# Performance work log

Hardware: AMD Instinct MI355X
Metric: run time of the kernel (lower is better)

The kernel has to match this reference:

```python
import jax, jax.numpy as jnp
import numpy as np

B, DX, DY = 64, 1024, 10

def setup_inputs() -> dict:
    key = jax.random.key(0)
    k1, k2 = jax.random.split(key)
    inputs = jax.random.normal(k1, (B, DX, DX), dtype=jnp.float32)
    rho = jax.random.normal(k2, (DX, DY, DX, DY), dtype=jnp.float32)
    return {"inputs": inputs, "rho": rho}

def reference(inputs, rho):
    # Original: rho_res = einsum('bik,klmn,bmo->bilon', inputs, rho, inputs)
    #           trace   = einsum('bijij->b', rho_res)   (full trace of rank-5 tensor)
    #           rho_y   = einsum('bijik->bjk', rho_res / trace)  (partial trace)
    # Equivalent without materializing the rank-5 intermediate:
    #   rho_y_un[b,j,k] = sum_{i,p,m} inputs[b,i,p] rho[p,j,m,k] inputs[b,m,i]
    #                   = sum_{m,p} (inputs @ inputs)[b,m,p] rho[p,j,m,k]
    #   trace[b] = sum_j rho_y_un[b,j,j]  (partial trace commutes with full trace)
    A = jnp.einsum('bmi,bip->bmp', inputs, inputs)          # [B, DX, DX]
    rho_y = jnp.einsum('bmp,pjmk->bjk', A, rho)             # [B, DY, DY]
    trace = jnp.trace(rho_y, axis1=-2, axis2=-1)            # [B]
    return rho_y / trace[:, None, None]
```

## Files before the change

kernel.cpp:

```cpp
#include <hip/hip_runtime.h>
#include <stdint.h>

#define DX 1024
#define NB 64
#define DY 10
#define NJK 100

typedef unsigned short ushort_t;
typedef __attribute__((ext_vector_type(8))) short short8;
typedef __attribute__((ext_vector_type(4))) float f32x4;
typedef __attribute__((ext_vector_type(16))) float f32x16;

#define VMCNT6 asm volatile("s_waitcnt vmcnt(6)" ::: "memory")
#define VMCNT5 asm volatile("s_waitcnt vmcnt(5)" ::: "memory")
#define VMCNT4 asm volatile("s_waitcnt vmcnt(4)" ::: "memory")
#define VMCNT0 asm volatile("s_waitcnt vmcnt(0)" ::: "memory")
#define LGKM0 asm volatile("s_waitcnt lgkmcnt(0)" ::: "memory")
#define CFENCE asm volatile("" ::: "memory")

__device__ __forceinline__ unsigned short f2bf(float f) {
  unsigned int u = __builtin_bit_cast(unsigned int, f);
  u += 0x7fffu + ((u >> 16) & 1u);
  return (unsigned short)(u >> 16);
}
__device__ __forceinline__ float bf2f(unsigned short h) {
  unsigned int u = ((unsigned int)h) << 16;
  return __builtin_bit_cast(float, u);
}
__device__ __forceinline__ void gload16(const void* g, void* l) {
  __builtin_amdgcn_global_load_lds((const __attribute__((address_space(1))) unsigned int*)g,
                                   (__attribute__((address_space(3))) unsigned int*)l, 16, 0, 0);
}

__launch_bounds__(256)
__global__ void p0_rho(const float* __restrict__ rho, ushort_t* __restrict__ R2,
                       float* __restrict__ S) {
  __shared__ ushort_t R_s[112 * 128];
  int p = blockIdx.x;
  int t = threadIdx.x;
  const float* rp = rho + (size_t)p * (DY * DX * DY);
  ushort_t* R2p = R2 + (size_t)p * (112 * 1024);
  int m = t >> 1, h = t & 1;

  for (int mc = 0; mc < 8; ++mc) {
    __syncthreads();
    float ssum = 0.f;
#pragma unroll
    for (int j = 0; j < DY; ++j) {
      const float* bj = rp + (size_t)j * (DX * DY) + (size_t)(mc * 128 + m) * DY;
      const float4 q = *(const float4*)(bj + h * 4);
      const float e = bj[8 + h];
      int rb = j * DY + h * 4;
      R_s[((rb + 0) * 128 + m) ^ (((rb + 0) & 15) << 3)] = f2bf(q.x);
      R_s[((rb + 1) * 128 + m) ^ (((rb + 1) & 15) << 3)] = f2bf(q.y);
      R_s[((rb + 2) * 128 + m) ^ (((rb + 2) & 15) << 3)] = f2bf(q.z);
      R_s[((rb + 3) * 128 + m) ^ (((rb + 3) & 15) << 3)] = f2bf(q.w);
      int r8 = j * DY + 8 + h;
      R_s[(r8 * 128 + m) ^ ((r8 & 15) << 3)] = f2bf(e);
      if (h == 0) {
        if (j == 0) ssum += q.x;
        if (j == 1) ssum += q.y;
        if (j == 2) ssum += q.z;
        if (j == 3) ssum += q.w;
        if (j == 8) ssum += e;
      } else {
        if (j == 4) ssum += q.x;
        if (j == 5) ssum += q.y;
        if (j == 6) ssum += q.z;
        if (j == 7) ssum += q.w;
        if (j == 9) ssum += e;
      }
    }
    ssum += __shfl_xor(ssum, 1, 64);
    if (h == 0) S[(size_t)p * DX + mc * 128 + m] = ssum;
    __syncthreads();
#pragma unroll
    for (int i = 0; i < 7; ++i) {
      int c = i * 256 + t;
      int row = c >> 4, sl = c & 15;
      uint4 v = make_uint4(0u, 0u, 0u, 0u);
      if (row < NJK) v = *(const uint4*)&R_s[(row * 128 + sl * 8) ^ ((row & 15) << 3)];
      *(uint4*)(R2p + (size_t)row * 1024 + mc * 128 + sl * 8) = v;
    }
  }
}

__launch_bounds__(256)
__global__ void p0_split(const float* __restrict__ X,
                         ushort_t* __restrict__ XHL, ushort_t* __restrict__ XtHL) {
  __shared__ float T[64][65];
  int blk = blockIdx.x;
  int bl = blk >> 8;
  int tt = blk & 255;
  int r0 = (tt >> 4) << 6;
  int c0 = (tt & 15) << 6;
  const float* Xb = X + (size_t)bl * DX * DX;
  int t = threadIdx.x;
  int r = t >> 4, c = t & 15;
#pragma unroll
  for (int s = 0; s < 4; ++s) {
    const float4 v = *(const float4*)(Xb + (size_t)(r0 + r + 16 * s) * DX + c0 + c * 4);
    T[r + 16 * s][c * 4 + 0] = v.x;
    T[r + 16 * s][c * 4 + 1] = v.y;
    T[r + 16 * s][c * 4 + 2] = v.z;
    T[r + 16 * s][c * 4 + 3] = v.w;
  }
  __syncthreads();
  int s8 = t & 7;
  int rw = t >> 3;
  int isLo = s8 >> 2, q = s8 & 3;
#pragma unroll
  for (int ktl = 0; ktl < 2; ++ktl) {
#pragma unroll
    for (int sp = 0; sp < 2; ++sp) {
      int loc = rw + sp * 32;
      {
        unsigned short hh8[8];
#pragma unroll
        for (int e = 0; e < 8; ++e) {
          float x = T[loc][ktl * 32 + q * 8 + e];
          unsigned short hh = f2bf(x);
          hh8[e] = isLo ? f2bf(x - bf2f(hh)) : hh;
        }
        int kt = (c0 >> 5) + ktl;
        size_t off = (((size_t)bl * 32 + kt) * 1024 + (r0 + loc)) * 64 + s8 * 8;
        uint4 v;
        v.x = (unsigned)hh8[0] | ((unsigned)hh8[1] << 16);
        v.y = (unsigned)hh8[2] | ((unsigned)hh8[3] << 16);
        v.z = (unsigned)hh8[4] | ((unsigned)hh8[5] << 16);
        v.w = (unsigned)hh8[6] | ((unsigned)hh8[7] << 16);
        *(uint4*)(XHL + off) = v;
      }
      {
        unsigned short hh8[8];
#pragma unroll
        for (int e = 0; e < 8; ++e) {
          float x = T[ktl * 32 + q * 8 + e][loc];
          unsigned short hh = f2bf(x);
          hh8[e] = isLo ? f2bf(x - bf2f(hh)) : hh;
        }
        int kt = (r0 >> 5) + ktl;
        size_t off = (((size_t)bl * 32 + kt) * 1024 + (c0 + loc)) * 64 + s8 * 8;
        uint4 v;
        v.x = (unsigned)hh8[0] | ((unsigned)hh8[1] << 16);
        v.y = (unsigned)hh8[2] | ((unsigned)hh8[3] << 16);
        v.z = (unsigned)hh8[4] | ((unsigned)hh8[5] << 16);
        v.w = (unsigned)hh8[6] | ((unsigned)hh8[7] << 16);
        *(uint4*)(XtHL + off) = v;
      }
    }
  }
}

__launch_bounds__(512, 2)
__global__ void k1_gemm(const ushort_t* __restrict__ XHL,
                        const ushort_t* __restrict__ XtHL,
                        const float* __restrict__ S,
                        ushort_t* __restrict__ Ahg,
                        float* __restrict__ part_tr, int bg) {
  __shared__ ushort_t lds[65536];
  int wg = blockIdx.x;
  int cpx = gridDim.x >> 3;
  int gt = (wg & 7) * cpx + (wg >> 3);
  int bl = gt >> 4, tile = gt & 15;
  int b = bg + bl;
  int m0 = (tile >> 2) << 8, p0 = (tile & 3) << 8;
  int t = threadIdx.x;
  int wv = t >> 6, lane = t & 63, l31 = lane & 31, hi8 = lane >> 5;
  int wm = (wv >> 2) << 7, wp = (wv & 3) << 6;

  f32x16 acc[4][2];
#pragma unroll
  for (int mi = 0; mi < 4; ++mi)
#pragma unroll
    for (int ni = 0; ni < 2; ++ni)
#pragma unroll
      for (int e = 0; e < 16; ++e) acc[mi][ni][e] = 0.f;

  int lam = lane >> 3;
  int lsl = (lane & 7) ^ lam;
  const ushort_t* Asrc = XHL + ((size_t)bl * 32 * 1024 + m0) * 64 + (size_t)lsl * 8;
  const ushort_t* Bsrc = XtHL + ((size_t)bl * 32 * 1024 + p0) * 64 + (size_t)lsl * 8;
  int ldsw = (t & ~63) * 8;

  auto stageA2 = [&](int kt, int half) {
    int buf = (kt & 1) << 15;
    size_t ko = (size_t)kt * 65536;
#pragma unroll
    for (int i = half * 2; i < half * 2 + 2; ++i) {
      int rr = (i << 6) + (wv << 3) + lam;
      gload16(Asrc + ko + (size_t)rr * 64, &lds[buf + (i << 12) + ldsw]);
    }
  };
  auto stageB2 = [&](int kt, int half) {
    int buf = (kt & 1) << 15;
    size_t ko = (size_t)kt * 65536;
#pragma unroll
    for (int i = half * 2; i < half * 2 + 2; ++i) {
      int rr = (i << 6) + (wv << 3) + lam;
      gload16(Bsrc + ko + (size_t)rr * 64, &lds[buf + 16384 + (i << 12) + ldsw]);
    }
  };
  auto readB = [&](int buf, int kc, short8* bh, short8* blo) {
#pragma unroll
    for (int ni = 0; ni < 2; ++ni) {
      int p = wp + (ni << 5) + l31;
      int rowb = buf + 16384 + p * 64;
      bh[ni] = *(const short8*)&lds[rowb + (((kc * 2 + hi8) ^ (p & 7)) << 3)];
      blo[ni] = *(const short8*)&lds[rowb + (((4 + kc * 2 + hi8) ^ (p & 7)) << 3)];
    }
  };
  auto readA2 = [&](int buf, int kc, int mi, short8& a, short8& l) {
    int m = wm + (mi << 5) + l31;
    int rowa = buf + m * 64;
    a = *(const short8*)&lds[rowa + (((kc * 2 + hi8) ^ (m & 7)) << 3)];
    l = *(const short8*)&lds[rowa + (((4 + kc * 2 + hi8) ^ (m & 7)) << 3)];
  };
  auto mfma6 = [&](int mi, const short8& a, const short8& l,
                   const short8* bh, const short8* blo) {
    __builtin_amdgcn_s_setprio(1);
#pragma unroll
    for (int ni = 0; ni < 2; ++ni) {
      acc[mi][ni] = __builtin_amdgcn_mfma_f32_32x32x16_bf16(a, bh[ni], acc[mi][ni], 0, 0, 0);
      acc[mi][ni] = __builtin_amdgcn_mfma_f32_32x32x16_bf16(a, blo[ni], acc[mi][ni], 0, 0, 0);
      acc[mi][ni] = __builtin_amdgcn_mfma_f32_32x32x16_bf16(l, bh[ni], acc[mi][ni], 0, 0, 0);
    }
    __builtin_amdgcn_s_setprio(0);
  };

  stageA2(0, 0);
  stageA2(0, 1);
  stageB2(0, 0);
  stageB2(0, 1);
  VMCNT0;
  __builtin_amdgcn_s_barrier();

#pragma unroll 1
  for (int kt = 0; kt < 32; ++kt) {
    int buf = (kt & 1) << 15;
    short8 bh[2], blo[2], a, l;
    readB(buf, 0, bh, blo);
    readA2(buf, 0, 0, a, l);
    if (kt < 31) stageA2(kt + 1, 0);
    CFENCE; __builtin_amdgcn_s_barrier(); LGKM0; __builtin_amdgcn_sched_barrier(0);
    mfma6(0, a, l, bh, blo);
    readA2(buf, 0, 1, a, l);
    if (kt < 31) stageA2(kt + 1, 1);
    CFENCE; __builtin_amdgcn_s_barrier(); LGKM0; __builtin_amdgcn_sched_barrier(0);
    mfma6(1, a, l, bh, blo);
    readA2(buf, 0, 2, a, l);
    if (kt < 31) stageB2(kt + 1, 0);
    CFENCE; __builtin_amdgcn_s_barrier(); LGKM0; __builtin_amdgcn_sched_barrier(0);
    mfma6(2, a, l, bh, blo);
    readA2(buf, 0, 3, a, l);
    if (kt < 31) stageB2(kt + 1, 1);
    CFENCE; __builtin_amdgcn_s_barrier(); LGKM0; __builtin_amdgcn_sched_barrier(0);
    mfma6(3, a, l, bh, blo);
    readB(buf, 1, bh, blo);
    readA2(buf, 1, 0, a, l);
    CFENCE; __builtin_amdgcn_s_barrier(); LGKM0; __builtin_amdgcn_sched_barrier(0);
    mfma6(0, a, l, bh, blo);
    readA2(buf, 1, 1, a, l);
    if (kt < 31) { VMCNT4; }
    CFENCE; __builtin_amdgcn_s_barrier(); LGKM0; __builtin_amdgcn_sched_barrier(0);
    mfma6(1, a, l, bh, blo);
    readA2(buf, 1, 2, a, l);
    CFENCE; __builtin_amdgcn_s_barrier(); LGKM0; __builtin_amdgcn_sched_barrier(0);
    mfma6(2, a, l, bh, blo);
    readA2(buf, 1, 3, a, l);
    VMCNT0;
    CFENCE; __builtin_amdgcn_s_barrier(); LGKM0; __builtin_amdgcn_sched_barrier(0);
    mfma6(3, a, l, bh, blo);
  }

  float tracc = 0.f;
#pragma unroll
  for (int mi = 0; mi < 4; ++mi)
#pragma unroll
    for (int ni = 0; ni < 2; ++ni) {
      int p = p0 + wp + (ni << 5) + l31;
#pragma unroll
      for (int rg = 0; rg < 4; ++rg) {
        int m = m0 + wm + (mi << 5) + 8 * rg + 4 * hi8;
        const float4 sv = *(const float4*)(S + (size_t)p * DX + m);
        tracc += acc[mi][ni][rg * 4 + 0] * sv.x + acc[mi][ni][rg * 4 + 1] * sv.y +
                 acc[mi][ni][rg * 4 + 2] * sv.z + acc[mi][ni][rg * 4 + 3] * sv.w;
      }
    }
#pragma unroll
  for (int off = 32; off > 0; off >>= 1) tracc += __shfl_xor(tracc, off, 64);
  __syncthreads();
  if (lane == 0) ((float*)lds)[wv] = tracc;
  __syncthreads();
  if (t == 0) {
    float s = 0.f;
    for (int i = 0; i < 8; ++i) s += ((float*)lds)[i];
    part_tr[b * 16 + tile] = s;
  }
  __syncthreads();

#pragma unroll
  for (int mi = 0; mi < 4; ++mi)
#pragma unroll
    for (int ni = 0; ni < 2; ++ni) {
      int p = wp + (ni << 5) + l31;
#pragma unroll
      for (int rg = 0; rg < 4; ++rg) {
        int m = wm + (mi << 5) + 8 * rg + 4 * hi8;
        unsigned int h0 = f2bf(acc[mi][ni][rg * 4 + 0]);
        unsigned int h1 = f2bf(acc[mi][ni][rg * 4 + 1]);
        unsigned int h2 = f2bf(acc[mi][ni][rg * 4 + 2]);
        unsigned int h3 = f2bf(acc[mi][ni][rg * 4 + 3]);
        int idx = p * 256 + (((m >> 3) ^ (p & 7)) << 3) + (m & 7);
        *(uint2*)&lds[idx] = make_uint2(h0 | (h1 << 16), h2 | (h3 << 16));
      }
    }
  __syncthreads();
#pragma unroll
  for (int i = 0; i < 16; ++i) {
    int cc = i * 512 + t;
    int row = cc >> 5, sl = cc & 31;
    int idx = row * 256 + ((sl ^ (row & 7)) << 3);
    uint4 v = *(const uint4*)&lds[idx];
    *(uint4*)(Ahg + ((size_t)(p0 + row) * NB + b) * DX + m0 + sl * 8) = v;
  }
}

__launch_bounds__(256)
__global__ void k2_contract(const ushort_t* __restrict__ R2,
                            const ushort_t* __restrict__ Ahg,
                            float* __restrict__ part_rho) {
  __shared__ ushort_t lds[22528];
  int p = blockIdx.x;
  int t = threadIdx.x;
  int wv = t >> 6, lane = t & 63, lr = lane & 15, lg = lane >> 4;
  const ushort_t* R2p = R2 + (size_t)p * (112 * 1024);
  const ushort_t* Ahp = Ahg + (size_t)p * (NB * DX);

  f32x4 acc[7];
#pragma unroll
  for (int n = 0; n < 7; ++n)
#pragma unroll
    for (int i = 0; i < 4; ++i) acc[n][i] = 0.f;

  auto stage = [&](int mc) {
    int buf = (mc & 1) * 11264;
#pragma unroll
    for (int i = 0; i < 2; ++i) {
      int c = i * 256 + t;
      int br = c >> 3, sl = c & 7;
      int lsl = sl ^ (br & 7);
      gload16(Ahp + (size_t)br * DX + mc * 64 + lsl * 8,
              &lds[buf + (i * 256 + (t & ~63)) * 8]);
    }
#pragma unroll
    for (int i = 0; i < 4; ++i) {
      int c = i * 256 + t;
      if (c < 896) {
        int row = c >> 3, sl = c & 7;
        int lsl = sl ^ (row & 7);
        gload16(R2p + (size_t)row * 1024 + mc * 64 + lsl * 8,
                &lds[buf + 4096 + (i * 256 + (t & ~63)) * 8]);
      }
    }
  };

  stage(0);
#pragma unroll 1
  for (int mc = 0; mc < 16; ++mc) {
    int buf = (mc & 1) * 11264;
    if (mc < 15) {
      stage(mc + 1);
      if (wv < 2) { VMCNT6; } else { VMCNT5; }
    } else {
      VMCNT0;
    }
    __builtin_amdgcn_s_barrier();
    CFENCE;
#pragma unroll
    for (int s = 0; s < 2; ++s) {
      int slot = s * 4 + lg;
      int ra = 16 * wv + lr;
      short8 af = *(const short8*)&lds[buf + ra * 64 + ((slot ^ (ra & 7)) << 3)];
      __builtin_amdgcn_s_setprio(1);
#pragma unroll
      for (int n = 0; n < 7; ++n) {
        int rb = 16 * n + lr;
        short8 bf = *(const short8*)&lds[buf + 4096 + rb * 64 + ((slot ^ (rb & 7)) << 3)];
        acc[n] = __builtin_amdgcn_mfma_f32_16x16x32_bf16(af, bf, acc[n], 0, 0, 0);
      }
      __builtin_amdgcn_s_setprio(0);
    }
    CFENCE;
    __builtin_amdgcn_s_barrier();
  }
#pragma unroll
  for (int n = 0; n < 7; ++n) {
    int col = 16 * n + lr;
    if (col < NJK) {
#pragma unroll
      for (int i = 0; i < 4; ++i) {
        int b_ = 16 * wv + lg * 4 + i;
        part_rho[((size_t)p * NB + b_) * NJK + col] = acc[n][i];
      }
    }
  }
}

__launch_bounds__(128)
__global__ void k3a(const float* __restrict__ part_rho, float* __restrict__ ws2) {
  int blk = blockIdx.x;
  int b = blk >> 1, h = blk & 1;
  int t = threadIdx.x;
  if (t >= NJK) return;
  float s = 0.f;
  for (int pp = 0; pp < 512; ++pp)
    s += part_rho[((size_t)(h * 512 + pp) * NB + b) * NJK + t];
  ws2[(size_t)(h * NB + b) * 128 + t] = s;
}

__launch_bounds__(128)
__global__ void k3b(const float* __restrict__ ws2, const float* __restrict__ part_tr,
                    float* __restrict__ out) {
  int b = blockIdx.x;
  int t = threadIdx.x;
  float tr = 0.f;
#pragma unroll
  for (int i = 0; i < 16; ++i) tr += part_tr[b * 16 + i];
  if (t < NJK) {
    float v = ws2[(size_t)b * 128 + t] + ws2[(size_t)(NB + b) * 128 + t];
    out[b * NJK + t] = v / tr;
  }
}

extern "C" void kernel_launch(void* const* d_in, const int* in_sizes, int n_in,
                              void* d_out, int out_size, void* d_ws, size_t ws_size,
                              hipStream_t stream) {
  const float* X = (const float*)d_in[0];
  const float* rho = (const float*)d_in[1];
  float* out = (float*)d_out;
  char* ws = (char*)d_ws;

  const size_t MB = 1048576ull;
  const size_t need_big = 868 * MB + 65536;
  const size_t need_small = 484 * MB + 65536;

  if (ws_size >= need_big) {
    ushort_t* XHL = (ushort_t*)(ws);
    ushort_t* XtHL = (ushort_t*)(ws + 256 * MB);
    ushort_t* Ahg = (ushort_t*)(ws + 512 * MB);
    ushort_t* R2 = (ushort_t*)(ws + 640 * MB);
    float* S = (float*)(ws + 864 * MB);
    float* part_tr = (float*)(ws + 868 * MB);
    float* part_rho = (float*)(ws);
    float* ws2 = (float*)(ws + 32 * MB);

    hipLaunchKernelGGL(p0_rho, dim3(1024), dim3(256), 0, stream, rho, R2, S);
    hipLaunchKernelGGL(p0_split, dim3(16384), dim3(256), 0, stream, X, XHL, XtHL);
    hipLaunchKernelGGL(k1_gemm, dim3(1024), dim3(512), 0, stream, XHL, XtHL, S, Ahg, part_tr, 0);
    hipLaunchKernelGGL(k2_contract, dim3(1024), dim3(256), 0, stream, R2, Ahg, part_rho);
    hipLaunchKernelGGL(k3a, dim3(128), dim3(128), 0, stream, part_rho, ws2);
    hipLaunchKernelGGL(k3b, dim3(64), dim3(128), 0, stream, ws2, part_tr, out);
  } else {
    ushort_t* XHL = (ushort_t*)(ws);
    ushort_t* XtHL = (ushort_t*)(ws + 64 * MB);
    ushort_t* Ahg = (ushort_t*)(ws + 128 * MB);
    ushort_t* R2 = (ushort_t*)(ws + 256 * MB);
    float* S = (float*)(ws + 480 * MB);
    float* part_tr = (float*)(ws + 484 * MB);
    float* part_rho = (float*)(ws);
    float* ws2 = (float*)(ws + 32 * MB);
    if (ws_size < need_small) return;

    hipLaunchKernelGGL(p0_rho, dim3(1024), dim3(256), 0, stream, rho, R2, S);
    for (int g = 0; g < 4; ++g) {
      hipLaunchKernelGGL(p0_split, dim3(4096), dim3(256), 0, stream,
                         X + (size_t)g * 16 * DX * DX, XHL, XtHL);
      hipLaunchKernelGGL(k1_gemm, dim3(256), dim3(512), 0, stream, XHL, XtHL, S, Ahg, part_tr, g * 16);
    }
    hipLaunchKernelGGL(k2_contract, dim3(1024), dim3(256), 0, stream, R2, Ahg, part_rho);
    hipLaunchKernelGGL(k3a, dim3(128), dim3(128), 0, stream, part_rho, ws2);
    hipLaunchKernelGGL(k3b, dim3(64), dim3(128), 0, stream, ws2, part_tr, out);
  }
}
```

Measured before the change: 730.8 us.

## Co-schedule rho packing with the GEMM and move trace computation into the contraction

The rho-to-bf16 packing now runs as extra workgroups in the same launch as the X·X GEMM, so the two independent stages can overlap instead of running in sequence. The trace reduction is taken out of the GEMM epilogue. The GEMM instead stores a bf16 low-residual copy of A (Alg) alongside the high part. Odd workgroups of the contraction kernel rebuild A from the high and low parts, dot it with S to form per-p partial traces, and k3b reduces those across 1024 entries. This removes a dependency of k1 on S and one launch, but adds an extra 128MB write and read of Alg and raises the workspace requirement.

```diff
diff --git a/kernel.cpp b/kernel.cpp
--- a/kernel.cpp
+++ b/kernel.cpp
@@ -32,57 +32,66 @@
                                    (__attribute__((address_space(3))) unsigned int*)l, 16, 0, 0);
 }
 
-__launch_bounds__(256)
-__global__ void p0_rho(const float* __restrict__ rho, ushort_t* __restrict__ R2,
-                       float* __restrict__ S) {
-  __shared__ ushort_t R_s[112 * 128];
-  int p = blockIdx.x;
-  int t = threadIdx.x;
+__device__ __forceinline__ void rho_work(int p, int t, const float* __restrict__ rho,
+                                         ushort_t* __restrict__ R2, float* __restrict__ S,
+                                         ushort_t* R_s) {
   const float* rp = rho + (size_t)p * (DY * DX * DY);
   ushort_t* R2p = R2 + (size_t)p * (112 * 1024);
-  int m = t >> 1, h = t & 1;
+  int m = (t & 255) >> 1, h = t & 1;
+  bool act = t < 256;
 
   for (int mc = 0; mc < 8; ++mc) {
     __syncthreads();
-    float ssum = 0.f;
-#pragma unroll
-    for (int j = 0; j < DY; ++j) {
-      const float* bj = rp + (size_t)j * (DX * DY) + (size_t)(mc * 128 + m) * DY;
-      const float4 q = *(const float4*)(bj + h * 4);
-      const float e = bj[8 + h];
-      int rb = j * DY + h * 4;
-      R_s[((rb + 0) * 128 + m) ^ (((rb + 0) & 15) << 3)] = f2bf(q.x);
-      R_s[((rb + 1) * 128 + m) ^ (((rb + 1) & 15) << 3)] = f2bf(q.y);
-      R_s[((rb + 2) * 128 + m) ^ (((rb + 2) & 15) << 3)] = f2bf(q.z);
-      R_s[((rb + 3) * 128 + m) ^ (((rb + 3) & 15) << 3)] = f2bf(q.w);
-      int r8 = j * DY + 8 + h;
-      R_s[(r8 * 128 + m) ^ ((r8 & 15) << 3)] = f2bf(e);
-      if (h == 0) {
-        if (j == 0) ssum += q.x;
-        if (j == 1) ssum += q.y;
-        if (j == 2) ssum += q.z;
-        if (j == 3) ssum += q.w;
-        if (j == 8) ssum += e;
-      } else {
-        if (j == 4) ssum += q.x;
-        if (j == 5) ssum += q.y;
-        if (j == 6) ssum += q.z;
-        if (j == 7) ssum += q.w;
-        if (j == 9) ssum += e;
-      }
-    }
-    ssum += __shfl_xor(ssum, 1, 64);
-    if (h == 0) S[(size_t)p * DX + mc * 128 + m] = ssum;
+    if (act) {
+      float ssum = 0.f;
+#pragma unroll
+      for (int j = 0; j < DY; ++j) {
+        const float* bj = rp + (size_t)j * (DX * DY) + (size_t)(mc * 128 + m) * DY;
+        const float4 q = *(const float4*)(bj + h * 4);
+        const float e = bj[8 + h];
+        int rb = j * DY + h * 4;
+        R_s[((rb + 0) * 128 + m) ^ (((rb + 0) & 15) << 3)] = f2bf(q.x);
+        R_s[((rb + 1) * 128 + m) ^ (((rb + 1) & 15) << 3)] = f2bf(q.y);
+        R_s[((rb + 2) * 128 + m) ^ (((rb + 2) & 15) << 3)] = f2bf(q.z);
+        R_s[((rb + 3) * 128 + m) ^ (((rb + 3) & 15) << 3)] = f2bf(q.w);
+        int r8 = j * DY + 8 + h;
+        R_s[(r8 * 128 + m) ^ ((r8 & 15) << 3)] = f2bf(e);
+        if (h == 0) {
+          if (j == 0) ssum += q.x;
+          if (j == 1) ssum += q.y;
+          if (j == 2) ssum += q.z;
+          if (j == 3) ssum += q.w;
+          if (j == 8) ssum += e;
+        } else {
+          if (j == 4) ssum += q.x;
+          if (j == 5) ssum += q.y;
+          if (j == 6) ssum += q.z;
+          if (j == 7) ssum += q.w;
+          if (j == 9) ssum += e;
+        }
+      }
+      ssum += __shfl_xor(ssum, 1, 64);
+      if (h == 0) S[(size_t)p * DX + mc * 128 + m] = ssum;
+    }
     __syncthreads();
-#pragma unroll
-    for (int i = 0; i < 7; ++i) {
-      int c = i * 256 + t;
-      int row = c >> 4, sl = c & 15;
-      uint4 v = make_uint4(0u, 0u, 0u, 0u);
-      if (row < NJK) v = *(const uint4*)&R_s[(row * 128 + sl * 8) ^ ((row & 15) << 3)];
-      *(uint4*)(R2p + (size_t)row * 1024 + mc * 128 + sl * 8) = v;
-    }
-  }
+    if (act) {
+#pragma unroll
+      for (int i = 0; i < 7; ++i) {
+        int c = i * 256 + (t & 255);
+        int row = c >> 4, sl = c & 15;
+        uint4 v = make_uint4(0u, 0u, 0u, 0u);
+        if (row < NJK) v = *(const uint4*)&R_s[(row * 128 + sl * 8) ^ ((row & 15) << 3)];
+        *(uint4*)(R2p + (size_t)row * 1024 + mc * 128 + sl * 8) = v;
+      }
+    }
+  }
+}
+
+__launch_bounds__(256)
+__global__ void p0_rho_k(const float* __restrict__ rho, ushort_t* __restrict__ R2,
+                         float* __restrict__ S) {
+  __shared__ ushort_t R_s[112 * 128];
+  rho_work(blockIdx.x, threadIdx.x, rho, R2, S, R_s);
 }
 
 __launch_bounds__(256)
@@ -152,15 +161,11 @@
   }
 }
 
-__launch_bounds__(512, 2)
-__global__ void k1_gemm(const ushort_t* __restrict__ XHL,
-                        const ushort_t* __restrict__ XtHL,
-                        const float* __restrict__ S,
-                        ushort_t* __restrict__ Ahg,
-                        float* __restrict__ part_tr, int bg) {
-  __shared__ ushort_t lds[65536];
-  int wg = blockIdx.x;
-  int cpx = gridDim.x >> 3;
+__device__ __forceinline__ void k1_body(ushort_t* lds, int wg, int cpx, int bg,
+                                        const ushort_t* __restrict__ XHL,
+                                        const ushort_t* __restrict__ XtHL,
+                                        ushort_t* __restrict__ Ahg,
+                                        ushort_t* __restrict__ Alg) {
   int gt = (wg & 7) * cpx + (wg >> 3);
   int bl = gt >> 4, tile = gt & 15;
   int b = bg + bl;
@@ -273,32 +278,7 @@
     mfma6(3, a, l, bh, blo);
   }
 
-  float tracc = 0.f;
-#pragma unroll
-  for (int mi = 0; mi < 4; ++mi)
-#pragma unroll
-    for (int ni = 0; ni < 2; ++ni) {
-      int p = p0 + wp + (ni << 5) + l31;
-#pragma unroll
-      for (int rg = 0; rg < 4; ++rg) {
-        int m = m0 + wm + (mi << 5) + 8 * rg + 4 * hi8;
-        const float4 sv = *(const float4*)(S + (size_t)p * DX + m);
-        tracc += acc[mi][ni][rg * 4 + 0] * sv.x + acc[mi][ni][rg * 4 + 1] * sv.y +
-                 acc[mi][ni][rg * 4 + 2] * sv.z + acc[mi][ni][rg * 4 + 3] * sv.w;
-      }
-    }
-#pragma unroll
-  for (int off = 32; off > 0; off >>= 1) tracc += __shfl_xor(tracc, off, 64);
   __syncthreads();
-  if (lane == 0) ((float*)lds)[wv] = tracc;
-  __syncthreads();
-  if (t == 0) {
-    float s = 0.f;
-    for (int i = 0; i < 8; ++i) s += ((float*)lds)[i];
-    part_tr[b * 16 + tile] = s;
-  }
-  __syncthreads();
-
 #pragma unroll
   for (int mi = 0; mi < 4; ++mi)
 #pragma unroll
@@ -324,15 +304,105 @@
     uint4 v = *(const uint4*)&lds[idx];
     *(uint4*)(Ahg + ((size_t)(p0 + row) * NB + b) * DX + m0 + sl * 8) = v;
   }
+  __syncthreads();
+#pragma unroll
+  for (int mi = 0; mi < 4; ++mi)
+#pragma unroll
+    for (int ni = 0; ni < 2; ++ni) {
+      int p = wp + (ni << 5) + l31;
+#pragma unroll
+      for (int rg = 0; rg < 4; ++rg) {
+        int m = wm + (mi << 5) + 8 * rg + 4 * hi8;
+        unsigned int l0, l1, l2, l3;
+        {
+          float a0 = acc[mi][ni][rg * 4 + 0], a1 = acc[mi][ni][rg * 4 + 1];
+          float a2 = acc[mi][ni][rg * 4 + 2], a3 = acc[mi][ni][rg * 4 + 3];
+          l0 = f2bf(a0 - bf2f(f2bf(a0)));
+          l1 = f2bf(a1 - bf2f(f2bf(a1)));
+          l2 = f2bf(a2 - bf2f(f2bf(a2)));
+          l3 = f2bf(a3 - bf2f(f2bf(a3)));
+        }
+        int idx = p * 256 + (((m >> 3) ^ (p & 7)) << 3) + (m & 7);
+        *(uint2*)&lds[idx] = make_uint2(l0 | (l1 << 16), l2 | (l3 << 16));
+      }
+    }
+  __syncthreads();
+#pragma unroll
+  for (int i = 0; i < 16; ++i) {
+    int cc = i * 512 + t;
+    int row = cc >> 5, sl = cc & 31;
+    int idx = row * 256 + ((sl ^ (row & 7)) << 3);
+    uint4 v = *(const uint4*)&lds[idx];
+    *(uint4*)(Alg + ((size_t)(p0 + row) * NB + b) * DX + m0 + sl * 8) = v;
+  }
+}
+
+__launch_bounds__(512, 2)
+__global__ void mega_k1_rho(const float* __restrict__ rho, ushort_t* __restrict__ R2,
+                            float* __restrict__ S,
+                            const ushort_t* __restrict__ XHL,
+                            const ushort_t* __restrict__ XtHL,
+                            ushort_t* __restrict__ Ahg, ushort_t* __restrict__ Alg) {
+  __shared__ ushort_t lds[65536];
+  int bid = blockIdx.x;
+  int g = bid >> 4, r = bid & 15;
+  if (r < 8) {
+    k1_body(lds, g * 8 + r, 128, 0, XHL, XtHL, Ahg, Alg);
+  } else {
+    rho_work(g * 8 + (r - 8), threadIdx.x, rho, R2, S, lds);
+  }
+}
+
+__launch_bounds__(512, 2)
+__global__ void k1_kernel(const ushort_t* __restrict__ XHL,
+                          const ushort_t* __restrict__ XtHL,
+                          ushort_t* __restrict__ Ahg, ushort_t* __restrict__ Alg, int bg) {
+  __shared__ ushort_t lds[65536];
+  k1_body(lds, blockIdx.x, gridDim.x >> 3, bg, XHL, XtHL, Ahg, Alg);
 }
 
 __launch_bounds__(256)
-__global__ void k2_contract(const ushort_t* __restrict__ R2,
-                            const ushort_t* __restrict__ Ahg,
-                            float* __restrict__ part_rho) {
+__global__ void k2_mega(const ushort_t* __restrict__ R2,
+                        const ushort_t* __restrict__ Ahg,
+                        const ushort_t* __restrict__ Alg,
+                        const float* __restrict__ S,
+                        float* __restrict__ part_rho, float* __restrict__ part_tr) {
   __shared__ ushort_t lds[22528];
-  int p = blockIdx.x;
+  __shared__ float red[256];
+  int bid = blockIdx.x;
   int t = threadIdx.x;
+
+  if (bid & 1) {
+    int p = bid >> 1;
+    int b = t >> 2, q = t & 3;
+    const ushort_t* ah = Ahg + ((size_t)p * NB + b) * DX + q * 256;
+    const ushort_t* al = Alg + ((size_t)p * NB + b) * DX + q * 256;
+    const float* sv = S + (size_t)p * DX + q * 256;
+    float ts = 0.f;
+#pragma unroll 4
+    for (int i = 0; i < 32; ++i) {
+      uint4 hv = *(const uint4*)(ah + i * 8);
+      uint4 lv = *(const uint4*)(al + i * 8);
+      float4 s0 = *(const float4*)(sv + i * 8);
+      float4 s1 = *(const float4*)(sv + i * 8 + 4);
+      unsigned hw[4] = {hv.x, hv.y, hv.z, hv.w};
+      unsigned lw[4] = {lv.x, lv.y, lv.z, lv.w};
+      float ss[8] = {s0.x, s0.y, s0.z, s0.w, s1.x, s1.y, s1.z, s1.w};
+#pragma unroll
+      for (int e = 0; e < 4; ++e) {
+        float a0 = bf2f((unsigned short)(hw[e] & 0xffff)) + bf2f((unsigned short)(lw[e] & 0xffff));
+        float a1 = bf2f((unsigned short)(hw[e] >> 16)) + bf2f((unsigned short)(lw[e] >> 16));
+        ts += a0 * ss[2 * e] + a1 * ss[2 * e + 1];
+      }
+    }
+    red[t] = ts;
+    __syncthreads();
+    if (t < 64)
+      part_tr[(size_t)p * NB + t] = red[4 * t] + red[4 * t + 1] + red[4 * t + 2] + red[4 * t + 3];
+    return;
+  }
+
+  int p = bid >> 1;
   int wv = t >> 6, lane = t & 63, lr = lane & 15, lg = lane >> 4;
   const ushort_t* R2p = R2 + (size_t)p * (112 * 1024);
   const ushort_t* Ahp = Ahg + (size_t)p * (NB * DX);
@@ -422,14 +492,20 @@
 __launch_bounds__(128)
 __global__ void k3b(const float* __restrict__ ws2, const float* __restrict__ part_tr,
                     float* __restrict__ out) {
+  __shared__ float red[128];
   int b = blockIdx.x;
   int t = threadIdx.x;
   float tr = 0.f;
-#pragma unroll
-  for (int i = 0; i < 16; ++i) tr += part_tr[b * 16 + i];
+  for (int pp = t; pp < 1024; pp += 128) tr += part_tr[(size_t)pp * NB + b];
+  red[t] = tr;
+  __syncthreads();
+  for (int off = 64; off > 0; off >>= 1) {
+    if (t < off) red[t] += red[t + off];
+    __syncthreads();
+  }
   if (t < NJK) {
     float v = ws2[(size_t)b * 128 + t] + ws2[(size_t)(NB + b) * 128 + t];
-    out[b * NJK + t] = v / tr;
+    out[b * NJK + t] = v / red[0];
   }
 }
 
@@ -442,43 +518,48 @@
   char* ws = (char*)d_ws;
 
   const size_t MB = 1048576ull;
-  const size_t need_big = 868 * MB + 65536;
-  const size_t need_small = 484 * MB + 65536;
+  const size_t need_big = 997 * MB;
+  const size_t need_small = 613 * MB;
 
   if (ws_size >= need_big) {
     ushort_t* XHL = (ushort_t*)(ws);
     ushort_t* XtHL = (ushort_t*)(ws + 256 * MB);
     ushort_t* Ahg = (ushort_t*)(ws + 512 * MB);
-    ushort_t* R2 = (ushort_t*)(ws + 640 * MB);
-    float* S = (float*)(ws + 864 * MB);
-    float* part_tr = (float*)(ws + 868 * MB);
+    ushort_t* Alg = (ushort_t*)(ws + 640 * MB);
+    ushort_t* R2 = (ushort_t*)(ws + 768 * MB);
+    float* S = (float*)(ws + 992 * MB);
+    float* part_tr = (float*)(ws + 996 * MB);
     float* part_rho = (float*)(ws);
     float* ws2 = (float*)(ws + 32 * MB);
 
-    hipLaunchKernelGGL(p0_rho, dim3(1024), dim3(256), 0, stream, rho, R2, S);
     hipLaunchKernelGGL(p0_split, dim3(16384), dim3(256), 0, stream, X, XHL, XtHL);
-    hipLaunchKernelGGL(k1_gemm, dim3(1024), dim3(512), 0, stream, XHL, XtHL, S, Ahg, part_tr, 0);
-    hipLaunchKernelGGL(k2_contract, dim3(1024), dim3(256), 0, stream, R2, Ahg, part_rho);
+    hipLaunchKernelGGL(mega_k1_rho, dim3(2048), dim3(512), 0, stream,
+                       rho, R2, S, XHL, XtHL, Ahg, Alg);
+    hipLaunchKernelGGL(k2_mega, dim3(2048), dim3(256), 0, stream,
+                       R2, Ahg, Alg, S, part_rho, part_tr);
     hipLaunchKernelGGL(k3a, dim3(128), dim3(128), 0, stream, part_rho, ws2);
     hipLaunchKernelGGL(k3b, dim3(64), dim3(128), 0, stream, ws2, part_tr, out);
   } else {
     ushort_t* XHL = (ushort_t*)(ws);
     ushort_t* XtHL = (ushort_t*)(ws + 64 * MB);
     ushort_t* Ahg = (ushort_t*)(ws + 128 * MB);
-    ushort_t* R2 = (ushort_t*)(ws + 256 * MB);
-    float* S = (float*)(ws + 480 * MB);
-    float* part_tr = (float*)(ws + 484 * MB);
+    ushort_t* Alg = (ushort_t*)(ws + 256 * MB);
+    ushort_t* R2 = (ushort_t*)(ws + 384 * MB);
+    float* S = (float*)(ws + 608 * MB);
+    float* part_tr = (float*)(ws + 612 * MB);
     float* part_rho = (float*)(ws);
     float* ws2 = (float*)(ws + 32 * MB);
     if (ws_size < need_small) return;
 
-    hipLaunchKernelGGL(p0_rho, dim3(1024), dim3(256), 0, stream, rho, R2, S);
+    hipLaunchKernelGGL(p0_rho_k, dim3(1024), dim3(256), 0, stream, rho, R2, S);
     for (int g = 0; g < 4; ++g) {
       hipLaunchKernelGGL(p0_split, dim3(4096), dim3(256), 0, stream,
                          X + (size_t)g * 16 * DX * DX, XHL, XtHL);
-      hipLaunchKernelGGL(k1_gemm, dim3(256), dim3(512), 0, stream, XHL, XtHL, S, Ahg, part_tr, g * 16);
-    }
-    hipLaunchKernelGGL(k2_contract, dim3(1024), dim3(256), 0, stream, R2, Ahg, part_rho);
+      hipLaunchKernelGGL(k1_kernel, dim3(256), dim3(512), 0, stream,
+                         XHL, XtHL, Ahg, Alg, g * 16);
+    }
+    hipLaunchKernelGGL(k2_mega, dim3(2048), dim3(256), 0, stream,
+                       R2, Ahg, Alg, S, part_rho, part_tr);
     hipLaunchKernelGGL(k3a, dim3(128), dim3(128), 0, stream, part_rho, ws2);
     hipLaunchKernelGGL(k3b, dim3(64), dim3(128), 0, stream, ws2, part_tr, out);
   }
```

After: 1.101 ms. 50.7% more time.
